# Optimization experiments

Measured on AMD Instinct MI355X. Metric: run time of the kernel, lower is better.

## Reference

```python
import jax, jax.numpy as jnp
import numpy as np

H = 128          # hidden_size
HEADS = 4
D = H // HEADS   # per-head channels (PyG GAT model: out_channels // heads, concat=True)
LAYERS = 2
NEG_SLOPE = 0.2
B, O, V, E = 1024, 20, 400, 840
N = 1 + O + V    # nodes per graph: head + objectives + values
FMIN = float(np.finfo(np.float32).min)


def _gat_conv(x, src, dst, W, a_src, a_dst, b, M):
    """PyG GATConv (v1): x [M,H], src/dst [Etot] (self loops included)."""
    xh = (x @ W).reshape(M, HEADS, D)                       # [M, heads, D]
    al_s = jnp.sum(xh * a_src, axis=-1)                     # [M, heads]
    al_d = jnp.sum(xh * a_dst, axis=-1)                     # [M, heads]
    e = jax.nn.leaky_relu(al_s[src] + al_d[dst], NEG_SLOPE)  # [Etot, heads]
    emax = jax.ops.segment_max(e, dst, num_segments=M)      # every node has a self loop
    ex = jnp.exp(e - emax[dst])
    denom = jax.ops.segment_sum(ex, dst, num_segments=M)
    alpha = ex / denom[dst]                                 # softmax over incoming edges
    out = jax.ops.segment_sum(alpha[:, :, None] * xh[src], dst, num_segments=M)
    return out.reshape(M, H) + b


def setup_inputs() -> dict:
    key = jax.random.key(0)
    ks = jax.random.split(key, 24)
    f = lambda k, shp, s=0.1: (jax.random.normal(k, shp, dtype=jnp.float32) * s)
    inp = {
        'head_node': jax.random.normal(ks[0], (B, 2), dtype=jnp.float32),
        'objective_nodes': jax.random.normal(ks[1], (B, O, 2), dtype=jnp.float32),
        'value_nodes': jax.random.normal(ks[2], (B, V, 5), dtype=jnp.float32),
        'accept_mask': jax.random.uniform(ks[3], (B, 2), dtype=jnp.float32),
        'edge_indices': jax.random.randint(ks[4], (B, 2, E), 0, N, dtype=jnp.int32),
        # encoders
        'We_head': f(ks[5], (2, H), 1.0), 'be_head': jnp.zeros((H,), jnp.float32),
        'We_obj': f(ks[6], (2, H), 1.0), 'be_obj': jnp.zeros((H,), jnp.float32),
        'We_val': f(ks[7], (5, H), 0.7), 'be_val': jnp.zeros((H,), jnp.float32),
        # GAT layers (stacked over LAYERS)
        'W_gat': f(ks[8], (LAYERS, H, H)),
        'a_src': f(ks[9], (LAYERS, HEADS, D)),
        'a_dst': f(ks[10], (LAYERS, HEADS, D)),
        'b_gat': jnp.zeros((LAYERS, H), jnp.float32),
        # output heads
        'W_acc': f(ks[11], (H, 2), 0.01), 'b_acc': jnp.zeros((2,), jnp.float32),
        'W_off': f(ks[12], (H, 1), 0.01), 'b_off': jnp.zeros((1,), jnp.float32),
        'W_vf': f(ks[13], (H, 1)), 'b_vf': jnp.zeros((1,), jnp.float32),
    }
    return inp


def reference(head_node, objective_nodes, value_nodes, accept_mask,
              We_head, be_head, We_obj, be_obj, We_val, be_val,
              W_gat, a_src, a_dst, b_gat,
              W_acc, b_acc, W_off, b_off, W_vf, b_vf,
              edge_indices):
    M = B * N
    # small linear encoders + ReLU
    h_head = jax.nn.relu(head_node @ We_head + be_head)              # [B,H]
    h_obj = jax.nn.relu(objective_nodes @ We_obj + be_obj)           # [B,O,H]
    h_val = jax.nn.relu(value_nodes @ We_val + be_val)               # [B,V,H]
    x = jnp.concatenate([h_head[:, None, :], h_obj, h_val], axis=1).reshape(M, H)
    # batch graphs: offset per-graph node indices, then add self loops
    off = (jnp.arange(B, dtype=jnp.int32) * N)[:, None]
    src = (edge_indices[:, 0, :] + off).reshape(-1)
    dst = (edge_indices[:, 1, :] + off).reshape(-1)
    loops = jnp.arange(M, dtype=jnp.int32)
    src = jnp.concatenate([src, loops])
    dst = jnp.concatenate([dst, loops])
    # GAT stack: ReLU between layers (BasicGNN act) and module applies ReLU after
    for l in range(LAYERS):
        x = _gat_conv(x, src, dst, W_gat[l], a_src[l], a_dst[l], b_gat[l], M)
        x = jax.nn.relu(x)
    h_out = x.reshape(B, N, H)
    h_head_out = h_out[:, 0, :]                                      # [B,H]
    h_val_out = h_out[:, -V:, :]                                     # [B,V,H]
    # masked accept head, offer head over value nodes, value function
    accept_inf_mask = jnp.maximum(jnp.log(accept_mask), FMIN)
    accept_logits = h_head_out @ W_acc + b_acc + accept_inf_mask     # [B,2]
    offer_logits = (h_val_out @ W_off + b_off)[..., 0]               # [B,V]
    vf = h_head_out @ W_vf + b_vf                                    # [B,1]
    # action_logits = cat(accept, offer); vf appended for a single output
    return jnp.concatenate([accept_logits, offer_logits, vf], axis=-1)
```

## Files before the change

kernel.cpp:

```cpp
#include <hip/hip_runtime.h>
#include <math.h>

#define Bb 1024
#define Oo 20
#define Vv 400
#define Ee 840
#define Nn 421
#define Mm (Bb*Nn)
#define Hh 128
#define XST 136
#define FMINF (-3.402823466e38f)

#define PREP_WCONV 16
#define PREP_CSR   1024
#define PREP_ENC   1684
#define ENC_STRIDE (PREP_ENC*512)

typedef __attribute__((ext_vector_type(8))) short bf8v;
typedef __attribute__((ext_vector_type(4))) float f4v;

__device__ __forceinline__ float lrelu(float x){ return x > 0.f ? x : 0.2f*x; }
__device__ __forceinline__ float bf2f(unsigned int lo16){
    union { unsigned int u; float f; } v; v.u = lo16 << 16; return v.f;
}
__device__ __forceinline__ float bf2fs(short s){ return bf2f((unsigned short)s); }
__device__ __forceinline__ unsigned short f2bf(float f){
    union { float f; unsigned int u; } v; v.f = f;
    unsigned int u = v.u;
    u += 0x7fffu + ((u >> 16) & 1u);
    return (unsigned short)(u >> 16);
}

__global__ __launch_bounds__(512) void prep(
    const float* __restrict__ Wg, unsigned short* __restrict__ Wt,
    const int* __restrict__ ei, int* __restrict__ row_ptr, int* __restrict__ colb,
    const float* __restrict__ hn, const float* __restrict__ on, const float* __restrict__ vn,
    const float* __restrict__ Wh, const float* __restrict__ bh,
    const float* __restrict__ Wo, const float* __restrict__ bo,
    const float* __restrict__ Wv, const float* __restrict__ bv,
    unsigned short* __restrict__ x)
{
    __shared__ __align__(16) unsigned char pool[7680];

    const int blk = blockIdx.x;
    const int tid = threadIdx.x;

    if (blk < PREP_WCONV){
        int idx = blk*512 + tid;
        int l = idx >> 12;
        int n = (idx >> 5) & 127;
        int k0 = (idx & 31) * 4;
        #pragma unroll
        for (int q = 0; q < 4; q++){
            int k = k0 + q;
            Wt[(size_t)l*16384 + n*128 + k] = f2bf(Wg[(size_t)l*16384 + k*128 + n]);
        }
        return;
    }
    if (blk < PREP_WCONV + PREP_CSR){
        unsigned int* keys = (unsigned int*)pool;
        int*          srcL = (int*)(pool + 4096);
        int b = blk - PREP_WCONV;
        const int* eb = ei + (size_t)b*2*Ee;
        for (int e = tid; e < Ee; e += 512){
            srcL[e] = eb[e];
            keys[e] = ((unsigned int)eb[Ee + e] << 10) | (unsigned int)e;
        }
        if (tid < 1024 - Ee) keys[Ee + tid] = 0xFFFFFFFFu;
        __syncthreads();
        for (int k = 2; k <= 1024; k <<= 1){
            for (int j = k >> 1; j > 0; j >>= 1){
                {
                    int i = tid, l = i ^ j;
                    if (l > i){
                        unsigned int a = keys[i], c = keys[l];
                        bool asc = ((i & k) == 0);
                        if (asc ? (a > c) : (a < c)){ keys[i] = c; keys[l] = a; }
                    }
                }
                {
                    int i = tid + 512, l = i ^ j;
                    if (l > i){
                        unsigned int a = keys[i], c = keys[l];
                        bool asc = ((i & k) == 0);
                        if (asc ? (a > c) : (a < c)){ keys[i] = c; keys[l] = a; }
                    }
                }
                __syncthreads();
            }
        }
        for (int i = tid; i < Ee; i += 512){
            unsigned int ky = keys[i];
            int d = (int)(ky >> 10), e = (int)(ky & 1023u);
            colb[b*Ee + i] = srcL[e] | (d << 16);
        }
        if (tid <= Nn){
            unsigned int target = (unsigned int)tid << 10;
            int lo = 0, hi = 1024;
            while (lo < hi){
                int mid = (lo + hi) >> 1;
                if (keys[mid] < target) lo = mid + 1; else hi = mid;
            }
            row_ptr[b*(Nn+1) + tid] = (lo > Ee) ? Ee : lo;
        }
        return;
    }
    {
        float* Wsh = (float*)pool;
        if (tid < 256) Wsh[tid] = Wh[tid];
        else           Wsh[tid] = Wo[tid - 256];
        for (int t = tid; t < 640; t += 512) Wsh[512 + t] = Wv[t];
        if (tid < 128){
            Wsh[1152 + tid] = bh[tid];
            Wsh[1280 + tid] = bo[tid];
            Wsh[1408 + tid] = bv[tid];
        }
        __syncthreads();

        int idx0 = (blk - PREP_WCONV - PREP_CSR)*512 + tid;
        #pragma unroll
        for (int it = 0; it < 8; it++){
            int idx = idx0 + it*ENC_STRIDE;
            int row = idx >> 4, seg = idx & 15;
            int b = row / Nn;
            int i = row - b*Nn;
            int c = seg*8;
            float acc[8];
            if (i == 0){
                float h0 = hn[b*2], h1 = hn[b*2+1];
                #pragma unroll
                for (int q = 0; q < 8; q++)
                    acc[q] = Wsh[1152 + c + q] + h0*Wsh[c + q] + h1*Wsh[128 + c + q];
            } else if (i < 1 + Oo){
                const float* in = on + ((size_t)b*Oo + (i-1))*2;
                float h0 = in[0], h1 = in[1];
                #pragma unroll
                for (int q = 0; q < 8; q++)
                    acc[q] = Wsh[1280 + c + q] + h0*Wsh[256 + c + q] + h1*Wsh[384 + c + q];
            } else {
                const float* in = vn + ((size_t)b*Vv + (i-1-Oo))*5;
                float v0 = in[0], v1 = in[1], v2 = in[2], v3 = in[3], v4 = in[4];
                #pragma unroll
                for (int q = 0; q < 8; q++){
                    acc[q] = Wsh[1408 + c + q]
                           + v0*Wsh[512 +           c + q] + v1*Wsh[512 + 128 + c + q]
                           + v2*Wsh[512 + 256 + c + q]     + v3*Wsh[512 + 384 + c + q]
                           + v4*Wsh[512 + 512 + c + q];
                }
            }
            uint4 pk;
            pk.x = ((unsigned int)f2bf(fmaxf(acc[1],0.f)) << 16) | f2bf(fmaxf(acc[0],0.f));
            pk.y = ((unsigned int)f2bf(fmaxf(acc[3],0.f)) << 16) | f2bf(fmaxf(acc[2],0.f));
            pk.z = ((unsigned int)f2bf(fmaxf(acc[5],0.f)) << 16) | f2bf(fmaxf(acc[4],0.f));
            pk.w = ((unsigned int)f2bf(fmaxf(acc[7],0.f)) << 16) | f2bf(fmaxf(acc[6],0.f));
            *(uint4*)(x + (size_t)row*Hh + c) = pk;
        }
    }
}

template<bool LAST>
__global__ __launch_bounds__(512,4) void gat_layer(
    const unsigned short* __restrict__ xin,
    unsigned short* __restrict__ xout,
    const unsigned short* __restrict__ Wt,
    const float* __restrict__ asr,
    const float* __restrict__ adt,
    const float* __restrict__ bg,
    const int* __restrict__ row_ptr,
    const int* __restrict__ colb,
    const float* __restrict__ Woff,
    const float* __restrict__ Wacc,
    const float* __restrict__ Wvf,
    float* __restrict__ partOff,
    float* __restrict__ partHead)
{
    __shared__ unsigned short xh_s[Nn*64];
    __shared__ float als_s[Nn*2], ald_s[Nn*2];
    __shared__ float as_s[64], ad_s[64], bias_s[64];
    __shared__ __align__(16) unsigned char UPool[16384];

    float* p_s    = (float*)UPool;
    float* pself  = (float*)(UPool + 6720);
    int*   colb_s = (int*)  (UPool + 10096);
    int*   rp_s   = (int*)  (UPool + 13456);

    const int lb   = ((int)blockIdx.x & 7)*256 + ((int)blockIdx.x >> 3);
    const int b    = lb >> 1;
    const int half = lb & 1;
    const int chb  = half*64;
    const int tid  = threadIdx.x;
    const size_t base = (size_t)b * Nn;
    const int lane = tid & 63, wave = tid >> 6;
    const int l15 = lane & 15, lhi = lane >> 4;

    #define XH_EL(n_, c_)  xh_s[((n_)<<6) | ((c_) ^ (((n_)&7)<<3))]
    #define XH_CH(n_, c8_) (*(const bf8v*)(xh_s + (((n_)<<6) | (((c8_) ^ ((n_)&7))<<3))))
    #define WS_FRAG(n_, k8_) (*(const bf8v*)((const unsigned short*)UPool + (((n_)<<7) | (((k8_) ^ ((n_)&7))<<3))))

    for (int c = tid; c < 1024; c += 512){
        int n = c >> 4, k8 = c & 15;
        unsigned short* dst = (unsigned short*)UPool + ((n<<7) | ((k8 ^ (n&7))<<3));
        *(uint4*)dst = *(const uint4*)(Wt + (size_t)(chb + n)*Hh + k8*8);
    }
    if (tid < 64)        as_s[tid]       = asr[chb + tid];
    else if (tid < 128)  ad_s[tid-64]    = adt[chb + tid-64];
    else if (tid < 192)  bias_s[tid-128] = bg [chb + tid-128];
    __syncthreads();

    {
        int rt = wave;
        bf8v afN[4];
        {
            int mrow = (rt<<4) + l15; if (mrow >= Nn) mrow = Nn - 1;
            const unsigned short* xr = xin + (base + mrow)*Hh + lhi*8;
            #pragma unroll
            for (int kc = 0; kc < 4; kc++) afN[kc] = *(const bf8v*)(xr + kc*32);
        }
        while (rt < 27){
            bf8v af[4];
            #pragma unroll
            for (int kc = 0; kc < 4; kc++) af[kc] = afN[kc];
            int rtN = rt + 8;
            if (rtN < 27){
                int mrow = (rtN<<4) + l15; if (mrow >= Nn) mrow = Nn - 1;
                const unsigned short* xr = xin + (base + mrow)*Hh + lhi*8;
                #pragma unroll
                for (int kc = 0; kc < 4; kc++) afN[kc] = *(const bf8v*)(xr + kc*32);
            }
            const int row0 = rt << 4;
            #pragma unroll
            for (int ns = 0; ns < 4; ns++){
                const int nn = ns*16 + l15;
                f4v acc = {0.f,0.f,0.f,0.f};
                #pragma unroll
                for (int kc = 0; kc < 4; kc++)
                    acc = __builtin_amdgcn_mfma_f32_16x16x32_bf16(af[kc], WS_FRAG(nn, kc*4 + lhi), acc, 0,0,0);
                #pragma unroll
                for (int r = 0; r < 4; r++){
                    int m = row0 + lhi*4 + r;
                    if (m < Nn) XH_EL(m, nn) = f2bf(acc[r]);
                }
            }
            rt = rtN;
        }
    }
    __syncthreads();

    for (int idx = tid; idx < Nn*2; idx += 512){
        int n = idx >> 1, h2 = idx & 1;
        float s = 0.f, d = 0.f;
        #pragma unroll
        for (int j = 0; j < 4; j++){
            bf8v xv = XH_CH(n, h2*4 + j);
            #pragma unroll
            for (int q = 0; q < 8; q++){
                float xf = bf2fs(xv[q]);
                s += xf * as_s[h2*32 + j*8 + q];
                d += xf * ad_s[h2*32 + j*8 + q];
            }
        }
        als_s[idx] = s; ald_s[idx] = d;
    }
    for (int e = tid; e < Ee; e += 512) colb_s[e] = colb[b*Ee + e];
    for (int i2 = tid; i2 <= Nn; i2 += 512) rp_s[i2] = row_ptr[b*(Nn+1) + i2];
    __syncthreads();

    for (int idx = tid; idx < Ee*2; idx += 512){
        int e = idx >> 1, h2 = idx & 1;
        int pk = colb_s[e];
        int s = pk & 0xffff, dd = pk >> 16;
        p_s[idx] = __expf(fminf(lrelu(als_s[s*2 + h2] + ald_s[dd*2 + h2]), 60.f));
    }
    for (int idx = tid; idx < Nn*2; idx += 512)
        pself[idx] = __expf(fminf(lrelu(als_s[idx] + ald_s[idx]), 60.f));
    __syncthreads();

    {
        const int grp = tid >> 2, lane4 = tid & 3;
        const int c80 = lane4*2;
        const int ch0 = lane4*16;
        const int h2  = lane4 >> 1;
        float wof[16];
        if (LAST){
            #pragma unroll
            for (int q = 0; q < 16; q++) wof[q] = Woff[chb + ch0 + q];
        }
        for (int n = grp; n < Nn; n += 128){
            float den = pself[n*2 + h2];
            float a[16];
            {
                bf8v xv0 = XH_CH(n, c80);
                bf8v xv1 = XH_CH(n, c80 + 1);
                #pragma unroll
                for (int q = 0; q < 8; q++){
                    a[q]     = den * bf2fs(xv0[q]);
                    a[8 + q] = den * bf2fs(xv1[q]);
                }
            }
            int rp0 = rp_s[n], rp1 = rp_s[n+1];
            for (int e = rp0; e < rp1; e++){
                int s = colb_s[e] & 0xffff;
                float p = p_s[e*2 + h2];
                bf8v sv0 = XH_CH(s, c80);
                bf8v sv1 = XH_CH(s, c80 + 1);
                den += p;
                #pragma unroll
                for (int q = 0; q < 8; q++){
                    a[q]     += p * bf2fs(sv0[q]);
                    a[8 + q] += p * bf2fs(sv1[q]);
                }
            }
            float inv = 1.f/den;
            float o[16];
            #pragma unroll
            for (int q = 0; q < 16; q++) o[q] = fmaxf(a[q]*inv + bias_s[ch0 + q], 0.f);
            if (!LAST){
                unsigned int pk[8];
                #pragma unroll
                for (int q2 = 0; q2 < 8; q2++)
                    pk[q2] = ((unsigned int)f2bf(o[q2*2+1]) << 16) | f2bf(o[q2*2]);
                unsigned short* dst = xout + (base + n)*Hh + chb + ch0;
                *(uint4*)dst       = make_uint4(pk[0],pk[1],pk[2],pk[3]);
                *(uint4*)(dst + 8) = make_uint4(pk[4],pk[5],pk[6],pk[7]);
            } else {
                if (n >= 1 + Oo){
                    float po = 0.f;
                    #pragma unroll
                    for (int q = 0; q < 16; q++) po += o[q]*wof[q];
                    po += __shfl_xor(po,1); po += __shfl_xor(po,2);
                    if (lane4 == 0) partOff[((size_t)b*Vv + (n - 1 - Oo))*2 + half] = po;
                } else if (n == 0){
                    float pa0 = 0.f, pa1 = 0.f, pvf = 0.f;
                    #pragma unroll
                    for (int q = 0; q < 16; q++){
                        int gc = chb + ch0 + q;
                        float ov = o[q];
                        pa0 += ov*Wacc[gc*2]; pa1 += ov*Wacc[gc*2+1]; pvf += ov*Wvf[gc];
                    }
                    pa0 += __shfl_xor(pa0,1); pa0 += __shfl_xor(pa0,2);
                    pa1 += __shfl_xor(pa1,1); pa1 += __shfl_xor(pa1,2);
                    pvf += __shfl_xor(pvf,1); pvf += __shfl_xor(pvf,2);
                    if (lane4 == 0){
                        partHead[b*6 + half*3 + 0] = pa0;
                        partHead[b*6 + half*3 + 1] = pa1;
                        partHead[b*6 + half*3 + 2] = pvf;
                    }
                }
            }
        }
    }
    #undef XH_EL
    #undef XH_CH
    #undef WS_FRAG
}

__global__ __launch_bounds__(128) void heads2(const float* __restrict__ partOff,
    const float* __restrict__ partHead, const float* __restrict__ am,
    const float* __restrict__ bacc, const float* __restrict__ boff,
    const float* __restrict__ bvf, float* __restrict__ out)
{
    int b = blockIdx.x, tid = threadIdx.x;
    float bo = boff[0];
    for (int v = tid; v < Vv; v += 128){
        const float* p = partOff + ((size_t)b*Vv + v)*2;
        out[(size_t)b*403 + 2 + v] = p[0] + p[1] + bo;
    }
    if (tid == 0){
        out[(size_t)b*403 + 0]   = partHead[b*6+0] + partHead[b*6+3] + bacc[0] + fmaxf(logf(am[b*2+0]), FMINF);
        out[(size_t)b*403 + 1]   = partHead[b*6+1] + partHead[b*6+4] + bacc[1] + fmaxf(logf(am[b*2+1]), FMINF);
        out[(size_t)b*403 + 402] = partHead[b*6+2] + partHead[b*6+5] + bvf[0];
    }
}

__global__ __launch_bounds__(512) void gat_fused(
    unsigned short* __restrict__ xg,
    const unsigned short* __restrict__ Wt,
    const float* __restrict__ asr, const float* __restrict__ adt,
    const float* __restrict__ bg,
    const int* __restrict__ row_ptr, const int* __restrict__ colb,
    const float* __restrict__ am,
    const float* __restrict__ Wacc, const float* __restrict__ bacc,
    const float* __restrict__ Woff, const float* __restrict__ boff,
    const float* __restrict__ Wvf,  const float* __restrict__ bvf,
    float* __restrict__ out)
{
    __shared__ unsigned short xh_s[Nn][XST];
    __shared__ float als_s[Nn][4];
    __shared__ float ald_s[Nn][4];
    __shared__ float as_s[Hh], ad_s[Hh], bias_s[Hh];
    __shared__ __align__(16) unsigned char UPool[32768];

    float* p_s    = (float*)UPool;
    float* pself  = (float*)(UPool + 13440);
    int*   colb_s = (int*)  (UPool + 20176);
    int*   rp_s   = (int*)  (UPool + 23536);

    const int b   = blockIdx.x;
    const int tid = threadIdx.x;
    const size_t base = (size_t)b * Nn;
    const int lane = tid & 63, wave = tid >> 6;
    const int l15 = lane & 15, lhi = lane >> 4;

    #define BFRAG(n_, kb_) (*(const bf8v*)(UPool + ((n_)<<8) + ((kb_) ^ (((n_)&7)<<4))))

    for (int l = 0; l < 2; l++){
        const unsigned short* Wl = Wt + (size_t)l*16384;
        for (int c = tid; c < 2048; c += 512){
            int n = c >> 4, ck = c & 15;
            int dstb = (n << 8) + ((ck*16) ^ ((n & 7) << 4));
            *(uint4*)(UPool + dstb) = *(const uint4*)(Wl + n*Hh + ck*8);
        }
        if (tid < Hh)        as_s[tid]        = asr[l*Hh + tid];
        else if (tid < 2*Hh) ad_s[tid-Hh]     = adt[l*Hh + tid-Hh];
        else if (tid < 3*Hh) bias_s[tid-2*Hh] = bg [l*Hh + tid-2*Hh];
        __syncthreads();

        {
            int rt = wave;
            bf8v afN[4];
            {
                int mrow = (rt<<4) + l15; if (mrow >= Nn) mrow = Nn - 1;
                const unsigned short* xr = xg + (base + mrow)*Hh + lhi*8;
                #pragma unroll
                for (int kc = 0; kc < 4; kc++) afN[kc] = *(const bf8v*)(xr + kc*32);
            }
            while (rt < 27){
                bf8v af[4];
                #pragma unroll
                for (int kc = 0; kc < 4; kc++) af[kc] = afN[kc];
                int rtN = rt + 8;
                if (rtN < 27){
                    int mrow = (rtN<<4) + l15; if (mrow >= Nn) mrow = Nn - 1;
                    const unsigned short* xr = xg + (base + mrow)*Hh + lhi*8;
                    #pragma unroll
                    for (int kc = 0; kc < 4; kc++) afN[kc] = *(const bf8v*)(xr + kc*32);
                }
                const int row0 = rt << 4;
                #pragma unroll
                for (int ct2 = 0; ct2 < 4; ct2++){
                    const int c0 = ct2*32;
                    const int n0 = c0 + l15, n1 = n0 + 16;
                    f4v acc0 = {0.f,0.f,0.f,0.f}, acc1 = {0.f,0.f,0.f,0.f};
                    #pragma unroll
                    for (int kc = 0; kc < 4; kc++){
                        const int kb = kc*64 + lhi*16;
                        acc0 = __builtin_amdgcn_mfma_f32_16x16x32_bf16(af[kc], BFRAG(n0, kb), acc0, 0,0,0);
                        acc1 = __builtin_amdgcn_mfma_f32_16x16x32_bf16(af[kc], BFRAG(n1, kb), acc1, 0,0,0);
                    }
                    #pragma unroll
                    for (int r = 0; r < 4; r++){
                        int m = row0 + lhi*4 + r;
                        if (m < Nn){
                            xh_s[m][n0] = f2bf(acc0[r]);
                            xh_s[m][n1] = f2bf(acc1[r]);
                        }
                    }
                }
                rt = rtN;
            }
        }
        __syncthreads();

        for (int idx = tid; idx < Nn*4; idx += 512){
            int n = idx >> 2, h = idx & 3;
            const unsigned short* xr = &xh_s[n][h*32];
            float s = 0.f, d = 0.f;
            #pragma unroll
            for (int c4 = 0; c4 < 4; c4++){
                bf8v xv = *(const bf8v*)(xr + c4*8);
                #pragma unroll
                for (int q = 0; q < 8; q++){
                    float xf = bf2fs(xv[q]);
                    s += xf * as_s[h*32 + c4*8 + q];
                    d += xf * ad_s[h*32 + c4*8 + q];
                }
            }
            als_s[n][h] = s; ald_s[n][h] = d;
        }
        for (int e = tid; e < Ee; e += 512) colb_s[e] = colb[b*Ee + e];
        for (int i2 = tid; i2 <= Nn; i2 += 512) rp_s[i2] = row_ptr[b*(Nn+1) + i2];
        __syncthreads();

        for (int idx = tid; idx < Nn*4; idx += 512){
            int n = idx >> 2, h = idx & 3;
            float aldh = ald_s[n][h];
            pself[idx] = __expf(fminf(lrelu(als_s[n][h] + aldh), 60.f));
            int rp0 = rp_s[n], rp1 = rp_s[n+1];
            for (int e = rp0; e < rp1; e++){
                int s = colb_s[e] & 0xffff;
                p_s[e*4 + h] = __expf(fminf(lrelu(als_s[s][h] + aldh), 60.f));
            }
        }
        __syncthreads();

        {
            const int ha  = l15 >> 2;
            const int ch0 = l15 * 8;
            for (int n0 = wave*4; n0 < Nn; n0 += 32){
                int n = n0 + lhi;
                if (n < Nn){
                    float den = pself[n*4 + ha];
                    bf8v xv = *(const bf8v*)&xh_s[n][ch0];
                    float a[8];
                    #pragma unroll
                    for (int q = 0; q < 8; q++) a[q] = den * bf2fs(xv[q]);
                    int rp0 = rp_s[n], rp1 = rp_s[n+1];
                    for (int e = rp0; e < rp1; e++){
                        int s = colb_s[e] & 0xffff;
                        float pC = p_s[e*4 + ha];
                        den += pC;
                        bf8v sv = *(const bf8v*)&xh_s[s][ch0];
                        #pragma unroll
                        for (int q = 0; q < 8; q++) a[q] += pC * bf2fs(sv[q]);
                    }
                    float inv = 1.f/den;
                    unsigned int pk[4];
                    #pragma unroll
                    for (int q2 = 0; q2 < 4; q2++){
                        float o0 = fmaxf(a[q2*2]  *inv + bias_s[ch0 + q2*2],     0.f);
                        float o1 = fmaxf(a[q2*2+1]*inv + bias_s[ch0 + q2*2 + 1], 0.f);
                        pk[q2] = ((unsigned int)f2bf(o1) << 16) | f2bf(o0);
                    }
                    *(uint4*)(xg + (base + n)*Hh + ch0) = make_uint4(pk[0],pk[1],pk[2],pk[3]);
                }
            }
        }
        __syncthreads();
    }

    {
        const int ch0 = l15 * 8;
        for (int v0 = wave*4; v0 < Vv; v0 += 32){
            int v = v0 + lhi;
            if (v < Vv){
                bf8v xv = *(const bf8v*)(xg + (base + 1 + Oo + v)*Hh + ch0);
                float s = 0.f;
                #pragma unroll
                for (int q = 0; q < 8; q++) s += bf2fs(xv[q]) * Woff[ch0 + q];
                s += __shfl_xor(s,1); s += __shfl_xor(s,2);
                s += __shfl_xor(s,4); s += __shfl_xor(s,8);
                if (l15 == 0) out[(size_t)b*403 + 2 + v] = s + boff[0];
            }
        }
        if (wave == 0){
            int k0 = lane*2;
            unsigned int uv = *(const unsigned int*)(xg + base*Hh + k0);
            float x0 = bf2f(uv & 0xffffu), x1 = bf2f(uv >> 16);
            float s0 = x0*Wacc[k0*2]     + x1*Wacc[(k0+1)*2];
            float s1 = x0*Wacc[k0*2 + 1] + x1*Wacc[(k0+1)*2 + 1];
            float s2 = x0*Wvf[k0]        + x1*Wvf[k0+1];
            #pragma unroll
            for (int t = 1; t < 64; t <<= 1){
                s0 += __shfl_xor(s0, t);
                s1 += __shfl_xor(s1, t);
                s2 += __shfl_xor(s2, t);
            }
            if (lane == 0){
                out[(size_t)b*403 + 0]   = s0 + bacc[0] + fmaxf(logf(am[b*2+0]), FMINF);
                out[(size_t)b*403 + 1]   = s1 + bacc[1] + fmaxf(logf(am[b*2+1]), FMINF);
                out[(size_t)b*403 + 402] = s2 + bvf[0];
            }
        }
    }
    #undef BFRAG
}

extern "C" void kernel_launch(void* const* d_in, const int* in_sizes, int n_in,
                              void* d_out, int out_size, void* d_ws, size_t ws_size,
                              hipStream_t stream)
{
    const float* head_node = (const float*)d_in[0];
    const float* obj  = (const float*)d_in[1];
    const float* val  = (const float*)d_in[2];
    const float* am   = (const float*)d_in[3];
    const int*   ei   = (const int*)  d_in[4];
    const float* Weh  = (const float*)d_in[5];
    const float* beh  = (const float*)d_in[6];
    const float* Weo  = (const float*)d_in[7];
    const float* beo  = (const float*)d_in[8];
    const float* Wev  = (const float*)d_in[9];
    const float* bev  = (const float*)d_in[10];
    const float* Wg   = (const float*)d_in[11];
    const float* asr  = (const float*)d_in[12];
    const float* adt  = (const float*)d_in[13];
    const float* bgat = (const float*)d_in[14];
    const float* Wacc = (const float*)d_in[15];
    const float* bacc = (const float*)d_in[16];
    const float* Woff = (const float*)d_in[17];
    const float* boff = (const float*)d_in[18];
    const float* Wvf  = (const float*)d_in[19];
    const float* bvf  = (const float*)d_in[20];

    const size_t xBytes  = (size_t)Mm*Hh*2;
    const size_t rpBytes = (size_t)Bb*(Nn+1)*4;
    const size_t cbBytes = (size_t)Bb*Ee*4;
    const size_t wtBytes = (size_t)2*Hh*Hh*2;
    const size_t poBytes = (size_t)Bb*Vv*2*4;
    const size_t phBytes = (size_t)Bb*6*4;
    const size_t needFast = 2*xBytes + rpBytes + cbBytes + wtBytes + poBytes + phBytes;

    char* ws = (char*)d_ws;
    unsigned short* x0 = (unsigned short*)ws;          ws += xBytes;
    const bool fast = (ws_size >= needFast);
    unsigned short* x1 = fast ? (unsigned short*)ws : x0;
    if (fast) ws += xBytes;
    int* row_ptr = (int*)ws;                           ws += rpBytes;
    int* colb    = (int*)ws;                           ws += cbBytes;
    unsigned short* WtB = (unsigned short*)ws;         ws += wtBytes;
    float* partOff  = (float*)ws;                      ws += poBytes;
    float* partHead = (float*)ws;                      ws += phBytes;

    prep<<<PREP_WCONV + PREP_CSR + PREP_ENC, 512, 0, stream>>>(
        Wg, WtB, ei, row_ptr, colb,
        head_node, obj, val, Weh, beh, Weo, beo, Wev, bev, x0);
    if (fast){
        gat_layer<false><<<2048, 512, 0, stream>>>(x0, x1, WtB, asr, adt, bgat,
                                                   row_ptr, colb, Woff, Wacc, Wvf,
                                                   partOff, partHead);
        gat_layer<true><<<2048, 512, 0, stream>>>(x1, x0, WtB + 16384, asr + Hh, adt + Hh, bgat + Hh,
                                                  row_ptr, colb, Woff, Wacc, Wvf,
                                                  partOff, partHead);
        heads2<<<Bb, 128, 0, stream>>>(partOff, partHead, am, bacc, boff, bvf, (float*)d_out);
    } else {
        gat_fused<<<Bb, 512, 0, stream>>>(x0, WtB, asr, adt, bgat, row_ptr, colb,
                                          am, Wacc, bacc, Woff, boff, Wvf, bvf,
                                          (float*)d_out);
    }
}
```

Measured before the change: 192.6 us.

## Compute attention logits via MFMA and widen per-thread aggregation to 32 channels

```diff
diff --git a/kernel.cpp b/kernel.cpp
--- a/kernel.cpp
+++ b/kernel.cpp
@@ -207,6 +207,18 @@
     else if (tid < 192)  bias_s[tid-128] = bg [chb + tid-128];
     __syncthreads();
 
+    bf8v bp0 = {0,0,0,0,0,0,0,0}, bp1 = {0,0,0,0,0,0,0,0};
+    {
+        const float* avec = (l15 & 1) ? ad_s : as_s;
+        if (l15 < 2){
+            #pragma unroll
+            for (int i = 0; i < 8; i++) bp0[i] = (short)f2bf(avec[lhi*8 + i]);
+        } else if (l15 < 4){
+            #pragma unroll
+            for (int i = 0; i < 8; i++) bp1[i] = (short)f2bf(avec[32 + lhi*8 + i]);
+        }
+    }
+
     {
         int rt = wave;
         bf8v afN[4];
@@ -246,20 +258,23 @@
     }
     __syncthreads();
 
-    for (int idx = tid; idx < Nn*2; idx += 512){
-        int n = idx >> 1, h2 = idx & 1;
-        float s = 0.f, d = 0.f;
-        #pragma unroll
-        for (int j = 0; j < 4; j++){
-            bf8v xv = XH_CH(n, h2*4 + j);
-            #pragma unroll
-            for (int q = 0; q < 8; q++){
-                float xf = bf2fs(xv[q]);
-                s += xf * as_s[h2*32 + j*8 + q];
-                d += xf * ad_s[h2*32 + j*8 + q];
-            }
-        }
-        als_s[idx] = s; ald_s[idx] = d;
+    for (int rt = wave; rt < 27; rt += 8){
+        const int row0 = rt << 4;
+        int nr = row0 + l15; if (nr >= Nn) nr = Nn - 1;
+        bf8v pa0 = XH_CH(nr, lhi);
+        bf8v pa1 = XH_CH(nr, 4 + lhi);
+        f4v pac = {0.f,0.f,0.f,0.f};
+        pac = __builtin_amdgcn_mfma_f32_16x16x32_bf16(pa0, bp0, pac, 0,0,0);
+        pac = __builtin_amdgcn_mfma_f32_16x16x32_bf16(pa1, bp1, pac, 0,0,0);
+        if (l15 < 4){
+            float* dp = (l15 & 1) ? ald_s : als_s;
+            int h2c = l15 >> 1;
+            #pragma unroll
+            for (int r = 0; r < 4; r++){
+                int m = row0 + lhi*4 + r;
+                if (m < Nn) dp[m*2 + h2c] = pac[r];
+            }
+        }
     }
     for (int e = tid; e < Ee; e += 512) colb_s[e] = colb[b*Ee + e];
     for (int i2 = tid; i2 <= Nn; i2 += 512) rp_s[i2] = row_ptr[b*(Nn+1) + i2];
@@ -276,25 +291,29 @@
     __syncthreads();
 
     {
-        const int grp = tid >> 2, lane4 = tid & 3;
-        const int c80 = lane4*2;
-        const int ch0 = lane4*16;
-        const int h2  = lane4 >> 1;
-        float wof[16];
+        const int grp = tid >> 1, lane2 = tid & 1;
+        const int c80 = lane2*4;
+        const int ch0 = lane2*32;
+        const int h2  = lane2;
+        float wof[32];
         if (LAST){
             #pragma unroll
-            for (int q = 0; q < 16; q++) wof[q] = Woff[chb + ch0 + q];
-        }
-        for (int n = grp; n < Nn; n += 128){
+            for (int q = 0; q < 32; q++) wof[q] = Woff[chb + ch0 + q];
+        }
+        for (int n = grp; n < Nn; n += 256){
             float den = pself[n*2 + h2];
-            float a[16];
+            float a[32];
             {
                 bf8v xv0 = XH_CH(n, c80);
                 bf8v xv1 = XH_CH(n, c80 + 1);
+                bf8v xv2 = XH_CH(n, c80 + 2);
+                bf8v xv3 = XH_CH(n, c80 + 3);
                 #pragma unroll
                 for (int q = 0; q < 8; q++){
-                    a[q]     = den * bf2fs(xv0[q]);
-                    a[8 + q] = den * bf2fs(xv1[q]);
+                    a[q]      = den * bf2fs(xv0[q]);
+                    a[8 + q]  = den * bf2fs(xv1[q]);
+                    a[16 + q] = den * bf2fs(xv2[q]);
+                    a[24 + q] = den * bf2fs(xv3[q]);
                 }
             }
             int rp0 = rp_s[n], rp1 = rp_s[n+1];
@@ -303,44 +322,50 @@
                 float p = p_s[e*2 + h2];
                 bf8v sv0 = XH_CH(s, c80);
                 bf8v sv1 = XH_CH(s, c80 + 1);
+                bf8v sv2 = XH_CH(s, c80 + 2);
+                bf8v sv3 = XH_CH(s, c80 + 3);
                 den += p;
                 #pragma unroll
                 for (int q = 0; q < 8; q++){
-                    a[q]     += p * bf2fs(sv0[q]);
-                    a[8 + q] += p * bf2fs(sv1[q]);
+                    a[q]      += p * bf2fs(sv0[q]);
+                    a[8 + q]  += p * bf2fs(sv1[q]);
+                    a[16 + q] += p * bf2fs(sv2[q]);
+                    a[24 + q] += p * bf2fs(sv3[q]);
                 }
             }
             float inv = 1.f/den;
-            float o[16];
-            #pragma unroll
-            for (int q = 0; q < 16; q++) o[q] = fmaxf(a[q]*inv + bias_s[ch0 + q], 0.f);
+            float o[32];
+            #pragma unroll
+            for (int q = 0; q < 32; q++) o[q] = fmaxf(a[q]*inv + bias_s[ch0 + q], 0.f);
             if (!LAST){
-                unsigned int pk[8];
-                #pragma unroll
-                for (int q2 = 0; q2 < 8; q2++)
+                unsigned int pk[16];
+                #pragma unroll
+                for (int q2 = 0; q2 < 16; q2++)
                     pk[q2] = ((unsigned int)f2bf(o[q2*2+1]) << 16) | f2bf(o[q2*2]);
                 unsigned short* dst = xout + (base + n)*Hh + chb + ch0;
-                *(uint4*)dst       = make_uint4(pk[0],pk[1],pk[2],pk[3]);
-                *(uint4*)(dst + 8) = make_uint4(pk[4],pk[5],pk[6],pk[7]);
+                *(uint4*)dst        = make_uint4(pk[0], pk[1], pk[2], pk[3]);
+                *(uint4*)(dst + 8)  = make_uint4(pk[4], pk[5], pk[6], pk[7]);
+                *(uint4*)(dst + 16) = make_uint4(pk[8], pk[9], pk[10],pk[11]);
+                *(uint4*)(dst + 24) = make_uint4(pk[12],pk[13],pk[14],pk[15]);
             } else {
                 if (n >= 1 + Oo){
                     float po = 0.f;
                     #pragma unroll
-                    for (int q = 0; q < 16; q++) po += o[q]*wof[q];
-                    po += __shfl_xor(po,1); po += __shfl_xor(po,2);
-                    if (lane4 == 0) partOff[((size_t)b*Vv + (n - 1 - Oo))*2 + half] = po;
+                    for (int q = 0; q < 32; q++) po += o[q]*wof[q];
+                    po += __shfl_xor(po, 1);
+                    if (lane2 == 0) partOff[((size_t)b*Vv + (n - 1 - Oo))*2 + half] = po;
                 } else if (n == 0){
                     float pa0 = 0.f, pa1 = 0.f, pvf = 0.f;
                     #pragma unroll
-                    for (int q = 0; q < 16; q++){
+                    for (int q = 0; q < 32; q++){
                         int gc = chb + ch0 + q;
                         float ov = o[q];
                         pa0 += ov*Wacc[gc*2]; pa1 += ov*Wacc[gc*2+1]; pvf += ov*Wvf[gc];
                     }
-                    pa0 += __shfl_xor(pa0,1); pa0 += __shfl_xor(pa0,2);
-                    pa1 += __shfl_xor(pa1,1); pa1 += __shfl_xor(pa1,2);
-                    pvf += __shfl_xor(pvf,1); pvf += __shfl_xor(pvf,2);
-                    if (lane4 == 0){
+                    pa0 += __shfl_xor(pa0, 1);
+                    pa1 += __shfl_xor(pa1, 1);
+                    pvf += __shfl_xor(pvf, 1);
+                    if (lane2 == 0){
                         partHead[b*6 + half*3 + 0] = pa0;
                         partHead[b*6 + half*3 + 1] = pa1;
                         partHead[b*6 + half*3 + 2] = pvf;
```

Measured after the change: 300.6 us. 56.0% more time.
